# Kernel optimization log

Measured on AMD Instinct MI355X. Metric: run time of the kernel, lower is better.

## Reference

```python
import jax, jax.numpy as jnp
import numpy as np

B, H, S, D = 2, 16, 2048, 64
DROPOUT_P = 0.1
INV_SCALE = 8.0  # sqrt(D), original: q.size(3) * k.size(-1)**-0.5


def setup_inputs() -> dict:
    key = jax.random.key(0)
    kq, kk, kv, km = jax.random.split(key, 4)
    query = jax.random.normal(kq, (B, H, S, D), dtype=jnp.float32)
    k_ = jax.random.normal(kk, (B, H, S, D), dtype=jnp.float32)
    value = jax.random.normal(kv, (B, H, S, D), dtype=jnp.float32)
    keep = jax.random.bernoulli(km, 1.0 - DROPOUT_P, (B, H, S, S))
    # torch train-mode dropout: keep-mask scaled by 1/(1-p)
    dropout_mask = keep.astype(jnp.float32) / (1.0 - DROPOUT_P)
    return {"query": query, "key": k_, "value": value, "dropout_mask": dropout_mask}


def reference(query, key, value, dropout_mask):
    # qk = q @ k^T, scaled by 1/sqrt(D)
    scores = jnp.einsum("bhqd,bhkd->bhqk", query, key) / INV_SCALE
    probs = jax.nn.softmax(scores, axis=-1)
    probs = probs * dropout_mask  # deterministic dropout
    out = jnp.einsum("bhqk,bhkd->bhqd", probs, value)
    return out
```

## Files before the change

kernel.cpp:

```cpp
#include <hip/hip_runtime.h>
#include <hip/hip_bf16.h>

typedef __attribute__((ext_vector_type(4))) float f32x4;
typedef __attribute__((ext_vector_type(8))) short s16x8;
typedef __attribute__((ext_vector_type(4))) short s16x4;

constexpr int S    = 2048;
constexpr int D    = 64;
constexpr int BH   = 32;
constexpr int QBLK = 64;
constexpr int KBLK = 128;
constexpr int NSL  = S / KBLK;

__device__ __forceinline__ short f2bf(float f) {
  union { float f; unsigned u; } x;
  x.f = f;
  unsigned r = x.u + 0x7fffu + ((x.u >> 16) & 1u);
  return (short)(r >> 16);
}

typedef const __attribute__((address_space(1))) unsigned int* as1_u32p;
typedef __attribute__((address_space(3))) unsigned int* as3_u32p;

__global__ __launch_bounds__(256) void prepass(const float* __restrict__ K,
                                               const float* __restrict__ V,
                                               short* __restrict__ Kb,
                                               short* __restrict__ Vt) {
  const int bid = blockIdx.x;
  const int tid = threadIdx.x;
  if (bid < BH * 32) {
    const int bh = bid >> 5, sl = bid & 31;
    const float* src = K + ((size_t)bh * S + (size_t)sl * 64) * D;
    short* dst = Kb + ((size_t)bh * S + (size_t)sl * 64) * D;
    #pragma unroll
    for (int c = 0; c < 2; ++c) {
      const int idx = tid * 2 + c;
      const int row = idx >> 3;
      const int ch  = idx & 7;
      const float* s = src + row * D + ch * 8;
      f32x4 a = *(const f32x4*)s, b = *(const f32x4*)(s + 4);
      s16x8 o;
      #pragma unroll
      for (int j = 0; j < 4; ++j) { o[j] = f2bf(a[j]); o[4 + j] = f2bf(b[j]); }
      *(s16x8*)(dst + row * D + ((ch ^ (row & 7)) * 8)) = o;
    }
  } else {
    __shared__ short tile[128][72];
    const int b2 = bid - BH * 32;
    const int bh = b2 >> 4, sl = b2 & 15;
    const float* src = V + ((size_t)bh * S + (size_t)sl * 128) * D;
    {
      const int row = tid >> 1;
      const int c0  = (tid & 1) * 32;
      #pragma unroll
      for (int q = 0; q < 8; ++q) {
        f32x4 a = *(const f32x4*)(src + row * D + c0 + q * 4);
        #pragma unroll
        for (int j = 0; j < 4; ++j) tile[row][c0 + q * 4 + j] = f2bf(a[j]);
      }
    }
    __syncthreads();
    short* dst = Vt + (size_t)bh * S * D + (size_t)sl * (D * KBLK);
    const int d = tid >> 2;
    #pragma unroll
    for (int cc = 0; cc < 4; ++cc) {
      const int c = (tid & 3) * 4 + cc;
      s16x8 o;
      #pragma unroll
      for (int j = 0; j < 8; ++j) o[j] = tile[c * 8 + j][d];
      *(s16x8*)(dst + d * KBLK + ((c ^ (d & 15)) * 8)) = o;
    }
  }
}

__global__ __launch_bounds__(256, 4)
void attn_fwd6(const float* __restrict__ Qg, const short* __restrict__ Kb,
               const short* __restrict__ Vt, const float* __restrict__ Mg,
               float* __restrict__ Og) {
  __shared__ alignas(16) short K_lds[KBLK][64];
  __shared__ alignas(16) short V_lds[D][KBLK];
  __shared__ alignas(16) short P_lds[4][16][64];

  const int tid  = threadIdx.x;
  const int wave = tid >> 6;
  const int lane = tid & 63;
  const int lq   = lane & 15;
  const int g    = lane >> 4;

  const int bh = blockIdx.x & (BH - 1);
  const int qt = blockIdx.x / BH;
  const size_t base = (size_t)bh * S * D;
  const int    qrow = qt * QBLK + wave * 16 + lq;
  const float* mrow = Mg + ((size_t)bh * S + qrow) * S + g * 4;

  s16x8 qf[2];
  {
    const float sc = 1.44269504088896340736f * 0.125f;
    const float* qp = Qg + base + (size_t)qrow * D + g * 8;
    #pragma unroll
    for (int h2 = 0; h2 < 2; ++h2) {
      f32x4 a = *(const f32x4*)(qp + h2 * 32);
      f32x4 b = *(const f32x4*)(qp + h2 * 32 + 4);
      #pragma unroll
      for (int j = 0; j < 4; ++j) {
        qf[h2][j]     = f2bf(a[j] * sc);
        qf[h2][4 + j] = f2bf(b[j] * sc);
      }
    }
  }

  f32x4 acc[4];
  #pragma unroll
  for (int dt = 0; dt < 4; ++dt) acc[dt] = (f32x4)0.0f;
  float m = -1e30f, lp = 0.0f;

  const char* kbase = (const char*)(Kb + base);
  const char* vbase = (const char*)(Vt + base);
  char* kl = (char*)&K_lds[0][0];
  char* vl = (char*)&V_lds[0][0];
  char* pl = (char*)&P_lds[wave][lq][0];

  #pragma unroll 1
  for (int it = 0; it < NSL; ++it) {
    __syncthreads();
    {
      const char* ks = kbase + (size_t)it * 16384;
      const char* vs = vbase + (size_t)it * 16384;
      #pragma unroll
      for (int i = 0; i < 4; ++i) {
        __builtin_amdgcn_global_load_lds((as1_u32p)(ks + i * 4096 + tid * 16),
                                         (as3_u32p)(kl + i * 4096 + tid * 16), 16, 0, 0);
        __builtin_amdgcn_global_load_lds((as1_u32p)(vs + i * 4096 + tid * 16),
                                         (as3_u32p)(vl + i * 4096 + tid * 16), 16, 0, 0);
      }
    }
    __syncthreads();

    f32x4 mk[8];
    {
      const float* mp = mrow + it * KBLK;
      #pragma unroll
      for (int t = 0; t < 8; ++t) mk[t] = *(const f32x4*)(mp + t * 16);
    }

    #pragma unroll
    for (int h = 0; h < 2; ++h) {
      f32x4 st[4];
      __builtin_amdgcn_s_setprio(1);
      #pragma unroll
      for (int t = 0; t < 4; ++t) {
        st[t] = (f32x4)0.0f;
        #pragma unroll
        for (int h2 = 0; h2 < 2; ++h2) {
          const s16x8 kf = *(const s16x8*)(kl + (h * 64 + t * 16 + lq) * 128 +
                                           (((h2 * 4 + g) ^ (lq & 7)) * 16));
          st[t] = __builtin_amdgcn_mfma_f32_16x16x32_bf16(kf, qf[h2], st[t], 0, 0, 0);
        }
      }
      __builtin_amdgcn_s_setprio(0);

      float mx = st[0][0];
      #pragma unroll
      for (int t = 0; t < 4; ++t)
        #pragma unroll
        for (int r = 0; r < 4; ++r) mx = fmaxf(mx, st[t][r]);
      if (!__all(mx <= m + 8.0f)) {
        float rm = fmaxf(mx, __shfl_xor(mx, 16));
        rm = fmaxf(rm, __shfl_xor(rm, 32));
        const float mn  = fmaxf(m, rm);
        const float fac = __builtin_amdgcn_exp2f(m - mn);
        lp *= fac;
        #pragma unroll
        for (int dt = 0; dt < 4; ++dt)
          #pragma unroll
          for (int r = 0; r < 4; ++r) acc[dt][r] *= fac;
        m = mn;
      }
      float ps = 0.0f;
      #pragma unroll
      for (int t = 0; t < 4; ++t)
        #pragma unroll
        for (int r = 0; r < 4; ++r) {
          st[t][r] = __builtin_amdgcn_exp2f(st[t][r] - m);
          ps += st[t][r];
        }
      lp += ps;

      #pragma unroll
      for (int t = 0; t < 4; ++t) {
        const f32x4 mkv = mk[h * 4 + t];
        s16x4 pk;
        #pragma unroll
        for (int r = 0; r < 4; ++r) pk[r] = f2bf(st[t][r] * mkv[r]);
        *(s16x4*)(pl + (((2 * t + (g >> 1)) ^ (lq & 7)) * 16) + (g & 1) * 8) = pk;
      }
      asm volatile("" ::: "memory");

      __builtin_amdgcn_s_setprio(1);
      #pragma unroll
      for (int kk = 0; kk < 2; ++kk) {
        const s16x8 pf = *(const s16x8*)(pl + (((4 * kk + g) ^ (lq & 7)) * 16));
        #pragma unroll
        for (int dt = 0; dt < 4; ++dt) {
          const s16x8 vf = *(const s16x8*)(vl + (dt * 16 + lq) * 256 +
                                           (((h * 8 + kk * 4 + g) ^ lq) * 16));
          acc[dt] = __builtin_amdgcn_mfma_f32_16x16x32_bf16(vf, pf, acc[dt], 0, 0, 0);
        }
      }
      __builtin_amdgcn_s_setprio(0);
      asm volatile("" ::: "memory");
    }
  }

  float l = lp + __shfl_xor(lp, 16);
  l += __shfl_xor(l, 32);
  const float inv_l = 1.0f / l;
  float* op = Og + base + (size_t)qrow * D;
  #pragma unroll
  for (int dt = 0; dt < 4; ++dt) {
    f32x4 o;
    #pragma unroll
    for (int r = 0; r < 4; ++r) o[r] = acc[dt][r] * inv_l;
    *(f32x4*)(op + dt * 16 + g * 4) = o;
  }
}

__global__ __launch_bounds__(256, 4)
void attn_fwd_fb(const float* __restrict__ Qg, const float* __restrict__ Kg,
                 const float* __restrict__ Vg, const float* __restrict__ Mg,
                 float* __restrict__ Og) {
  __shared__ alignas(16) short Kl[32][72];
  __shared__ alignas(16) short Vl[D][40];
  __shared__ alignas(16) short Pl[4][16][40];
  const int tid = threadIdx.x, wave = tid >> 6, lane = tid & 63;
  const int lq = lane & 15, g = lane >> 4;
  const int bh = blockIdx.x & (BH - 1), qt = blockIdx.x / BH;
  const size_t base = (size_t)bh * S * D;
  const int qrow = qt * QBLK + wave * 16 + lq;
  const float* mrow = Mg + ((size_t)bh * S + qrow) * S;
  s16x8 qf[2];
  {
    const float sc = 1.44269504088896340736f * 0.125f;
    const float* qp = Qg + base + (size_t)qrow * D + g * 8;
    #pragma unroll
    for (int h = 0; h < 2; ++h) {
      f32x4 a = *(const f32x4*)(qp + h * 32);
      f32x4 b = *(const f32x4*)(qp + h * 32 + 4);
      #pragma unroll
      for (int j = 0; j < 4; ++j) { qf[h][j] = f2bf(a[j] * sc); qf[h][4 + j] = f2bf(b[j] * sc); }
    }
  }
  f32x4 acc[4];
  #pragma unroll
  for (int dt = 0; dt < 4; ++dt) acc[dt] = (f32x4)0.0f;
  float m = -1e30f, l = 0.0f;
  for (int kb = 0; kb < S; kb += 32) {
    f32x4 mk[2];
    #pragma unroll
    for (int t = 0; t < 2; ++t) mk[t] = *(const f32x4*)(mrow + kb + t * 16 + g * 4);
    __syncthreads();
    {
      const int row = tid >> 3, d0 = (tid & 7) * 8;
      const float* kp = Kg + base + (size_t)(kb + row) * D + d0;
      f32x4 a = *(const f32x4*)kp, b = *(const f32x4*)(kp + 4);
      s16x8 f;
      #pragma unroll
      for (int j = 0; j < 4; ++j) { f[j] = f2bf(a[j]); f[4 + j] = f2bf(b[j]); }
      *(s16x8*)&Kl[row][d0] = f;
    }
    {
      const int d = tid & 63, kk = (tid >> 6) * 8;
      const float* vp = Vg + base + (size_t)(kb + kk) * D + d;
      s16x8 f;
      #pragma unroll
      for (int j = 0; j < 8; ++j) f[j] = f2bf(vp[(size_t)j * D]);
      *(s16x8*)&Vl[d][kk] = f;
    }
    __syncthreads();
    f32x4 st[2];
    #pragma unroll
    for (int t = 0; t < 2; ++t) {
      st[t] = (f32x4)0.0f;
      #pragma unroll
      for (int h = 0; h < 2; ++h) {
        s16x8 kf = *(const s16x8*)&Kl[t * 16 + lq][h * 32 + g * 8];
        st[t] = __builtin_amdgcn_mfma_f32_16x16x32_bf16(kf, qf[h], st[t], 0, 0, 0);
      }
    }
    float mx = st[0][0];
    #pragma unroll
    for (int t = 0; t < 2; ++t)
      #pragma unroll
      for (int r = 0; r < 4; ++r) mx = fmaxf(mx, st[t][r]);
    mx = fmaxf(mx, __shfl_xor(mx, 16));
    mx = fmaxf(mx, __shfl_xor(mx, 32));
    const float mn = fmaxf(m, mx);
    const float fac = __builtin_amdgcn_exp2f(m - mn);
    float p[8], ps = 0.0f;
    #pragma unroll
    for (int t = 0; t < 2; ++t)
      #pragma unroll
      for (int r = 0; r < 4; ++r) { float e = __builtin_amdgcn_exp2f(st[t][r] - mn); p[t * 4 + r] = e; ps += e; }
    ps += __shfl_xor(ps, 16);
    ps += __shfl_xor(ps, 32);
    l = l * fac + ps; m = mn;
    #pragma unroll
    for (int dt = 0; dt < 4; ++dt)
      #pragma unroll
      for (int r = 0; r < 4; ++r) acc[dt][r] *= fac;
    #pragma unroll
    for (int t = 0; t < 2; ++t) {
      s16x4 pk;
      #pragma unroll
      for (int r = 0; r < 4; ++r) pk[r] = f2bf(p[t * 4 + r] * mk[t][r]);
      *(s16x4*)&Pl[wave][lq][t * 16 + g * 4] = pk;
    }
    asm volatile("" ::: "memory");
    s16x8 pf = *(const s16x8*)&Pl[wave][lq][g * 8];
    #pragma unroll
    for (int dt = 0; dt < 4; ++dt) {
      s16x8 vf = *(const s16x8*)&Vl[dt * 16 + lq][g * 8];
      acc[dt] = __builtin_amdgcn_mfma_f32_16x16x32_bf16(vf, pf, acc[dt], 0, 0, 0);
    }
  }
  const float inv_l = 1.0f / l;
  float* op = Og + base + (size_t)qrow * D;
  #pragma unroll
  for (int dt = 0; dt < 4; ++dt) {
    f32x4 o;
    #pragma unroll
    for (int r = 0; r < 4; ++r) o[r] = acc[dt][r] * inv_l;
    *(f32x4*)(op + dt * 16 + g * 4) = o;
  }
}

extern "C" void kernel_launch(void* const* d_in, const int* in_sizes, int n_in,
                              void* d_out, int out_size, void* d_ws, size_t ws_size,
                              hipStream_t stream) {
  const float* Q = (const float*)d_in[0];
  const float* K = (const float*)d_in[1];
  const float* V = (const float*)d_in[2];
  const float* M = (const float*)d_in[3];
  float* O = (float*)d_out;
  const size_t need = 2ull * BH * S * D * sizeof(short);
  if (ws_size >= need) {
    short* Kb = (short*)d_ws;
    short* Vt = Kb + (size_t)BH * S * D;
    prepass<<<BH * 32 + BH * 16, 256, 0, stream>>>(K, V, Kb, Vt);
    attn_fwd6<<<(S / QBLK) * BH, 256, 0, stream>>>(Q, Kb, Vt, M, O);
  } else {
    attn_fwd_fb<<<(S / QBLK) * BH, 256, 0, stream>>>(Q, K, V, M, O);
  }
}
```

Before: 158.7 us.

## Rotate KV tile order per block, issue mask loads before barrier, use builtin bf16 convert

Each block now starts its K/V/mask tile loop at a rotated offset derived from query tile and head, so concurrent blocks hit different K/V slices and spread memory-channel traffic. The dropout-mask register loads are issued before the barrier that waits for the LDS fill, so both sets of loads are in flight together. The hand-written round-to-nearest bf16 conversion is replaced with the HIP __float2bfloat16 intrinsic, which may lower to hardware convert instructions. Softmax is order-independent under online rescaling, so results change only by rounding order.

```diff
diff --git a/kernel.cpp b/kernel.cpp
--- a/kernel.cpp
+++ b/kernel.cpp
@@ -12,11 +12,10 @@
 constexpr int KBLK = 128;
 constexpr int NSL  = S / KBLK;
 
-__device__ __forceinline__ short f2bf(float f) {
-  union { float f; unsigned u; } x;
-  x.f = f;
-  unsigned r = x.u + 0x7fffu + ((x.u >> 16) & 1u);
-  return (short)(r >> 16);
+__device__ __forceinline__ short bf16c(float f) {
+  __hip_bfloat16 h = __float2bfloat16(f);
+  union { __hip_bfloat16 h; short s; } u; u.h = h;
+  return u.s;
 }
 
 typedef const __attribute__((address_space(1))) unsigned int* as1_u32p;
@@ -41,7 +40,7 @@
       f32x4 a = *(const f32x4*)s, b = *(const f32x4*)(s + 4);
       s16x8 o;
       #pragma unroll
-      for (int j = 0; j < 4; ++j) { o[j] = f2bf(a[j]); o[4 + j] = f2bf(b[j]); }
+      for (int j = 0; j < 4; ++j) { o[j] = bf16c(a[j]); o[4 + j] = bf16c(b[j]); }
       *(s16x8*)(dst + row * D + ((ch ^ (row & 7)) * 8)) = o;
     }
   } else {
@@ -56,7 +55,7 @@
       for (int q = 0; q < 8; ++q) {
         f32x4 a = *(const f32x4*)(src + row * D + c0 + q * 4);
         #pragma unroll
-        for (int j = 0; j < 4; ++j) tile[row][c0 + q * 4 + j] = f2bf(a[j]);
+        for (int j = 0; j < 4; ++j) tile[row][c0 + q * 4 + j] = bf16c(a[j]);
       }
     }
     __syncthreads();
@@ -74,9 +73,9 @@
 }
 
 __global__ __launch_bounds__(256, 4)
-void attn_fwd6(const float* __restrict__ Qg, const short* __restrict__ Kb,
-               const short* __restrict__ Vt, const float* __restrict__ Mg,
-               float* __restrict__ Og) {
+void attn_fwd12(const float* __restrict__ Qg, const short* __restrict__ Kb,
+                const short* __restrict__ Vt, const float* __restrict__ Mg,
+                float* __restrict__ Og) {
   __shared__ alignas(16) short K_lds[KBLK][64];
   __shared__ alignas(16) short V_lds[D][KBLK];
   __shared__ alignas(16) short P_lds[4][16][64];
@@ -92,6 +91,7 @@
   const size_t base = (size_t)bh * S * D;
   const int    qrow = qt * QBLK + wave * 16 + lq;
   const float* mrow = Mg + ((size_t)bh * S + qrow) * S + g * 4;
+  const int    rot  = (qt + bh) & (NSL - 1);
 
   s16x8 qf[2];
   {
@@ -103,8 +103,8 @@
       f32x4 b = *(const f32x4*)(qp + h2 * 32 + 4);
       #pragma unroll
       for (int j = 0; j < 4; ++j) {
-        qf[h2][j]     = f2bf(a[j] * sc);
-        qf[h2][4 + j] = f2bf(b[j] * sc);
+        qf[h2][j]     = bf16c(a[j] * sc);
+        qf[h2][4 + j] = bf16c(b[j] * sc);
       }
     }
   }
@@ -122,10 +122,11 @@
 
   #pragma unroll 1
   for (int it = 0; it < NSL; ++it) {
-    __syncthreads();
-    {
-      const char* ks = kbase + (size_t)it * 16384;
-      const char* vs = vbase + (size_t)it * 16384;
+    const int ip = (it + rot) & (NSL - 1);
+    __syncthreads();
+    {
+      const char* ks = kbase + (size_t)ip * 16384;
+      const char* vs = vbase + (size_t)ip * 16384;
       #pragma unroll
       for (int i = 0; i < 4; ++i) {
         __builtin_amdgcn_global_load_lds((as1_u32p)(ks + i * 4096 + tid * 16),
@@ -134,14 +135,13 @@
                                          (as3_u32p)(vl + i * 4096 + tid * 16), 16, 0, 0);
       }
     }
-    __syncthreads();
-
     f32x4 mk[8];
     {
-      const float* mp = mrow + it * KBLK;
+      const float* mp = mrow + ip * KBLK;
       #pragma unroll
       for (int t = 0; t < 8; ++t) mk[t] = *(const f32x4*)(mp + t * 16);
     }
+    __syncthreads();
 
     #pragma unroll
     for (int h = 0; h < 2; ++h) {
@@ -191,7 +191,7 @@
         const f32x4 mkv = mk[h * 4 + t];
         s16x4 pk;
         #pragma unroll
-        for (int r = 0; r < 4; ++r) pk[r] = f2bf(st[t][r] * mkv[r]);
+        for (int r = 0; r < 4; ++r) pk[r] = bf16c(st[t][r] * mkv[r]);
         *(s16x4*)(pl + (((2 * t + (g >> 1)) ^ (lq & 7)) * 16) + (g & 1) * 8) = pk;
       }
       asm volatile("" ::: "memory");
@@ -247,7 +247,7 @@
       f32x4 a = *(const f32x4*)(qp + h * 32);
       f32x4 b = *(const f32x4*)(qp + h * 32 + 4);
       #pragma unroll
-      for (int j = 0; j < 4; ++j) { qf[h][j] = f2bf(a[j] * sc); qf[h][4 + j] = f2bf(b[j] * sc); }
+      for (int j = 0; j < 4; ++j) { qf[h][j] = bf16c(a[j] * sc); qf[h][4 + j] = bf16c(b[j] * sc); }
     }
   }
   f32x4 acc[4];
@@ -265,7 +265,7 @@
       f32x4 a = *(const f32x4*)kp, b = *(const f32x4*)(kp + 4);
       s16x8 f;
       #pragma unroll
-      for (int j = 0; j < 4; ++j) { f[j] = f2bf(a[j]); f[4 + j] = f2bf(b[j]); }
+      for (int j = 0; j < 4; ++j) { f[j] = bf16c(a[j]); f[4 + j] = bf16c(b[j]); }
       *(s16x8*)&Kl[row][d0] = f;
     }
     {
@@ -273,7 +273,7 @@
       const float* vp = Vg + base + (size_t)(kb + kk) * D + d;
       s16x8 f;
       #pragma unroll
-      for (int j = 0; j < 8; ++j) f[j] = f2bf(vp[(size_t)j * D]);
+      for (int j = 0; j < 8; ++j) f[j] = bf16c(vp[(size_t)j * D]);
       *(s16x8*)&Vl[d][kk] = f;
     }
     __syncthreads();
@@ -312,7 +312,7 @@
     for (int t = 0; t < 2; ++t) {
       s16x4 pk;
       #pragma unroll
-      for (int r = 0; r < 4; ++r) pk[r] = f2bf(p[t * 4 + r] * mk[t][r]);
+      for (int r = 0; r < 4; ++r) pk[r] = bf16c(p[t * 4 + r] * mk[t][r]);
       *(s16x4*)&Pl[wave][lq][t * 16 + g * 4] = pk;
     }
     asm volatile("" ::: "memory");
@@ -342,12 +342,13 @@
   const float* V = (const float*)d_in[2];
   const float* M = (const float*)d_in[3];
   float* O = (float*)d_out;
-  const size_t need = 2ull * BH * S * D * sizeof(short);
+  const size_t nKV = (size_t)BH * S * D;
+  const size_t need = 2 * nKV * sizeof(short);
   if (ws_size >= need) {
     short* Kb = (short*)d_ws;
-    short* Vt = Kb + (size_t)BH * S * D;
+    short* Vt = Kb + nKV;
     prepass<<<BH * 32 + BH * 16, 256, 0, stream>>>(K, V, Kb, Vt);
-    attn_fwd6<<<(S / QBLK) * BH, 256, 0, stream>>>(Q, Kb, Vt, M, O);
+    attn_fwd12<<<(S / QBLK) * BH, 256, 0, stream>>>(Q, Kb, Vt, M, O);
   } else {
     attn_fwd_fb<<<(S / QBLK) * BH, 256, 0, stream>>>(Q, K, V, M, O);
   }
```

Result: faster. 147.2 us (-7.3%).
